# Kernel optimization log

Hardware: AMD Instinct MI355X
Metric: run time of the kernel (lower is better)

Reference implementation:

```python
import jax, jax.numpy as jnp
import numpy as np

LOG2 = float(np.log(2.0))

def ssp(v):
    # ShiftedSoftplus: softplus(x) - log(2)
    return jax.nn.softplus(v) - jnp.asarray(LOG2, v.dtype)

def setup_inputs() -> dict:
    key = jax.random.key(0)
    ks = jax.random.split(key, 16)
    N, B, F, R, P = 100000, 128, 64, 32, 1600000
    inp = {
        "x": jax.random.normal(ks[0], (N, B), jnp.float32),
        "f_ij": jax.random.uniform(ks[1], (P, R), jnp.float32),
        "rcut_ij": jax.random.uniform(ks[2], (P,), jnp.float32),
        "pairlist": jax.random.randint(ks[3], (2, P), 0, N, jnp.int64),
        # input_to_feature: Linear(B, F)
        "w_in": jax.random.normal(ks[4], (B, F), jnp.float32) * (1.0 / np.sqrt(B)),
        "b_in": jnp.zeros((F,), jnp.float32),
        # filter_network: Linear(R, F) + SSP, Linear(F, F)
        "w_f1": jax.random.normal(ks[5], (R, F), jnp.float32) * (1.0 / np.sqrt(R)),
        "b_f1": jnp.zeros((F,), jnp.float32),
        "w_f2": jax.random.normal(ks[6], (F, F), jnp.float32) * (1.0 / np.sqrt(F)),
        "b_f2": jnp.zeros((F,), jnp.float32),
        # feature_to_output: Linear(F, B) + SSP, Linear(B, B)
        "w_o1": jax.random.normal(ks[7], (F, B), jnp.float32) * (1.0 / np.sqrt(F)),
        "b_o1": jnp.zeros((B,), jnp.float32),
        "w_o2": jax.random.normal(ks[8], (B, B), jnp.float32) * (1.0 / np.sqrt(B)),
        "b_o2": jnp.zeros((B,), jnp.float32),
    }
    return inp

def reference(x, f_ij, rcut_ij, pairlist, w_in, b_in, w_f1, b_f1, w_f2, b_f2, w_o1, b_o1, w_o2, b_o2):
    n_atoms = x.shape[0]
    # input_to_feature
    h = x @ w_in + b_in                                    # [N, F]
    # filter_network on rbf features, weighted by cutoff
    Wij = ssp(f_ij @ w_f1 + b_f1) @ w_f2 + b_f2            # [P, F]
    Wij = Wij * rcut_ij[:, None]
    idx_i, idx_j = pairlist[0], pairlist[1]
    # gather neighbor features, modulate, scatter-add to center atoms
    x_ij = h[idx_j] * Wij                                  # [P, F]
    agg = jax.ops.segment_sum(x_ij, idx_i, num_segments=n_atoms)  # [N, F]
    # feature_to_output
    out = ssp(agg @ w_o1 + b_o1) @ w_o2 + b_o2             # [N, B]
    return out
```

## Files before the change

kernel.cpp:

```cpp
#include <hip/hip_runtime.h>
#include <hip/hip_bf16.h>
#include <hip/hip_fp16.h>

#define B_ 128
#define F_ 64
#define R_ 32

typedef __attribute__((ext_vector_type(8))) __bf16 bf16x8;
typedef __attribute__((ext_vector_type(4))) float f32x4;

#define LN2F 0.6931471805599453f
#define L2EF 1.4426950408889634f

__device__ __forceinline__ float sspf(float x) {
    float t = fabsf(x) * (-L2EF);
    float e; asm("v_exp_f32 %0, %1" : "=v"(e) : "v"(t));
    float l; asm("v_log_f32 %0, %1" : "=v"(l) : "v"(1.0f + e));
    return fmaxf(x, 0.0f) + fmaf(LN2F, l, -LN2F);
}
__device__ __forceinline__ float bfbits2f(unsigned int us) { return __uint_as_float(us << 16); }
__device__ __forceinline__ unsigned int f2bf(float f) {
    unsigned int u = __float_as_uint(f);
    return (u + 0x7fffu + ((u >> 16) & 1u)) >> 16;
}
__device__ __forceinline__ float h16f(unsigned short s) { return __half2float(__ushort_as_half(s)); }
__device__ __forceinline__ unsigned int pkbf(float a, float b) {
    __hip_bfloat162 h = __float22bfloat162_rn(make_float2(a, b));
    unsigned int r; __builtin_memcpy(&r, &h, 4); return r;
}
__device__ __forceinline__ unsigned int pkh(float a, float b) {
    __half2 h = __float22half2_rn(make_float2(a, b));
    unsigned int r; __builtin_memcpy(&r, &h, 4); return r;
}

__global__ __launch_bounds__(256) void front_kernel(
    const float* __restrict__ w1, const float* __restrict__ w2,
    const float* __restrict__ wo1, const float* __restrict__ wo2,
    unsigned short* __restrict__ w1p, unsigned short* __restrict__ w2p,
    unsigned short* __restrict__ wo1p, unsigned short* __restrict__ wo2p,
    const void* __restrict__ pl, int* __restrict__ flag, int P,
    const float* __restrict__ x, const float* __restrict__ w_in,
    const float* __restrict__ b_in, unsigned short* __restrict__ h, int NA,
    int* __restrict__ hist, int hgrid)
{
    int b = blockIdx.x;
    if (b < 15) {
        int t = b * 256 + threadIdx.x;
        if (t < 256) {
            int ct = t >> 6, l = t & 63, g = l >> 4, m = l & 15;
            #pragma unroll
            for (int i = 0; i < 8; ++i)
                w1p[t * 8 + i] = (unsigned short)f2bf(w1[(g * 8 + i) * F_ + ct * 16 + m]);
        } else if (t < 768) {
            int q = t - 256;
            int kh = q >> 8, ct = (q >> 6) & 3, l = q & 63, g = l >> 4, m = l & 15;
            #pragma unroll
            for (int i = 0; i < 8; ++i)
                w2p[q * 8 + i] = (unsigned short)f2bf(w2[(kh * 32 + g * 8 + i) * F_ + ct * 16 + m]);
        } else if (t < 2816) {
            int q = t - 768;
            int l = q & 63, ct = (q >> 6) & 3, kh = (q >> 8) & 3, ch = q >> 10;
            int g = l >> 4, m = l & 15;
            #pragma unroll
            for (int i = 0; i < 8; ++i)
                wo2p[q * 8 + i] = (unsigned short)f2bf(wo2[(kh * 32 + g * 8 + i) * B_ + ch * 64 + ct * 16 + m]);
        } else if (t < 3840) {
            int q = t - 2816;
            int l = q & 63, ct = (q >> 6) & 3, kh = (q >> 8) & 1, ch = q >> 9;
            int g = l >> 4, m = l & 15;
            #pragma unroll
            for (int i = 0; i < 8; ++i)
                wo1p[q * 8 + i] = (unsigned short)f2bf(wo1[(kh * 32 + g * 8 + i) * B_ + ch * 64 + ct * 16 + m]);
        }
        return;
    }
    if (b == 15) {
        if (threadIdx.x < 64) {
            int n = (P < 64) ? P : 64;
            const long long* p64 = (const long long*)pl;
            bool bad = false;
            if ((int)threadIdx.x < n) {
                long long v = p64[threadIdx.x];
                bad = (v < 0) || (v >= 100000000LL);
            }
            unsigned long long bl = __ballot(bad);
            if (threadIdx.x == 0) *flag = (bl == 0ULL) ? 1 : 0;
        }
        return;
    }
    if (b < 16 + hgrid) {
        int n = (b - 16) * 256 + threadIdx.x;
        if (n >= NA) return;
        float acc[F_];
        #pragma unroll
        for (int f = 0; f < F_; ++f) acc[f] = b_in[f];
        const float4* xrow = (const float4*)(x + (size_t)n * B_);
        #pragma unroll 2
        for (int rb = 0; rb < B_ / 4; ++rb) {
            float4 xv = xrow[rb];
            const float* w0 = w_in + (size_t)(4 * rb) * F_;
            #pragma unroll
            for (int f = 0; f < F_; ++f) acc[f] = fmaf(xv.x, w0[f], acc[f]);
            #pragma unroll
            for (int f = 0; f < F_; ++f) acc[f] = fmaf(xv.y, w0[F_ + f], acc[f]);
            #pragma unroll
            for (int f = 0; f < F_; ++f) acc[f] = fmaf(xv.z, w0[2 * F_ + f], acc[f]);
            #pragma unroll
            for (int f = 0; f < F_; ++f) acc[f] = fmaf(xv.w, w0[3 * F_ + f], acc[f]);
        }
        uint4* hrow = (uint4*)(h + (size_t)n * F_);
        #pragma unroll
        for (int q = 0; q < F_ / 8; ++q) {
            uint4 ob;
            ob.x = pkbf(acc[8 * q + 0], acc[8 * q + 1]);
            ob.y = pkbf(acc[8 * q + 2], acc[8 * q + 3]);
            ob.z = pkbf(acc[8 * q + 4], acc[8 * q + 5]);
            ob.w = pkbf(acc[8 * q + 6], acc[8 * q + 7]);
            hrow[q] = ob;
        }
        return;
    }
    __shared__ int sflag;
    if (threadIdx.x < 64) {
        int n = (P < 64) ? P : 64;
        const long long* p64 = (const long long*)pl;
        bool bad = false;
        if ((int)threadIdx.x < n) {
            long long v = p64[threadIdx.x];
            bad = (v < 0) || (v >= 100000000LL);
        }
        unsigned long long bl = __ballot(bad);
        if (threadIdx.x == 0) sflag = (bl == 0ULL) ? 1 : 0;
    }
    __syncthreads();
    int p = (b - 16 - hgrid) * 256 + threadIdx.x;
    if (p >= P) return;
    int i = sflag ? (int)((const long long*)pl)[p] : ((const int*)pl)[p];
    atomicAdd(&hist[i], 1);
}

__global__ __launch_bounds__(256) void scan1_kernel(
    const int* __restrict__ hist, int* __restrict__ off,
    int* __restrict__ bsum, int NA)
{
    __shared__ int s[256];
    int t = threadIdx.x;
    int idx = blockIdx.x * 2048 + t * 8;
    int v[8];
    int run = 0;
    #pragma unroll
    for (int k = 0; k < 8; ++k) {
        int i = idx + k;
        int c = (i < NA) ? hist[i] : 0;
        v[k] = run; run += c;
    }
    s[t] = run;
    __syncthreads();
    for (int o = 1; o < 256; o <<= 1) {
        int x = (t >= o) ? s[t - o] : 0;
        __syncthreads();
        s[t] += x;
        __syncthreads();
    }
    int base = (t == 0) ? 0 : s[t - 1];
    #pragma unroll
    for (int k = 0; k < 8; ++k) {
        int i = idx + k;
        if (i < NA) off[i] = v[k] + base;
    }
    if (t == 255) bsum[blockIdx.x] = s[255];
}

__global__ __launch_bounds__(256) void scan2_kernel(int* __restrict__ bsum, int nb) {
    __shared__ int s[256];
    int t = threadIdx.x;
    int v = (t < nb) ? bsum[t] : 0;
    s[t] = v;
    __syncthreads();
    for (int o = 1; o < 256; o <<= 1) {
        int x = (t >= o) ? s[t - o] : 0;
        __syncthreads();
        s[t] += x;
        __syncthreads();
    }
    if (t < nb) bsum[t] = s[t] - v;
}

__global__ __launch_bounds__(256) void scan3_kernel(
    int* __restrict__ off, int* __restrict__ cursor,
    const int* __restrict__ bsum, int NA, int P)
{
    int i = blockIdx.x * 256 + threadIdx.x;
    if (i > NA) return;
    if (i == NA) { off[NA] = P; return; }
    int v = off[i] + bsum[i >> 11];
    off[i] = v;
    cursor[i] = v;
}

template <bool ATOMIC>
__global__ __launch_bounds__(256, 4) void pair_kernel(
    const float* __restrict__ f_ij, const float* __restrict__ rcut,
    const void* __restrict__ pl, const int* __restrict__ flag,
    const unsigned short* __restrict__ w1p, const float* __restrict__ b1,
    const unsigned short* __restrict__ w2p, const float* __restrict__ b2,
    const unsigned short* __restrict__ h, unsigned short* __restrict__ xs,
    int* __restrict__ cursor, int* __restrict__ jslot,
    float* __restrict__ agg_f32, int P)
{
    __shared__ __align__(16) unsigned short T[256 * 64];
    __shared__ __align__(16) int   ii[256];
    __shared__ __align__(16) int   jj[256];
    __shared__ __align__(16) float rr[256];

    const int tid   = threadIdx.x;
    const int lane  = tid & 63;
    const int wv    = tid >> 6;
    const int g     = lane >> 4;
    const int m     = lane & 15;
    const int pbase = blockIdx.x * 256;
    const int wbase = wv * 64;

    {
        int p = pbase + tid;
        bool valid = (p < P);
        int pc = valid ? p : (P > 0 ? P - 1 : 0);
        long long i_, j_;
        if (*flag) {
            const long long* p64 = (const long long*)pl;
            i_ = p64[pc]; j_ = p64[(size_t)P + pc];
        } else {
            const int* p32 = (const int*)pl;
            i_ = p32[pc]; j_ = p32[(size_t)P + pc];
        }
        jj[tid] = valid ? (int)j_ : 0;
        rr[tid] = valid ? rcut[pc] : 0.0f;
        if (ATOMIC) {
            ii[tid] = valid ? (int)i_ : 0;
        } else {
            int pos = valid ? atomicAdd(&cursor[(int)i_], 1) : (P + tid);
            ii[tid] = pos;
            if (valid) jslot[pos] = (int)j_;
        }
    }

    bf16x8 w1f[4], w2f[2][4];
    #pragma unroll
    for (int ct = 0; ct < 4; ++ct)
        w1f[ct] = *(const bf16x8*)&w1p[(ct * 64 + lane) * 8];
    #pragma unroll
    for (int kh = 0; kh < 2; ++kh)
        #pragma unroll
        for (int ct = 0; ct < 4; ++ct)
            w2f[kh][ct] = *(const bf16x8*)&w2p[((kh * 4 + ct) * 64 + lane) * 8];

    float4 b1v[4], b2v[4];
    #pragma unroll
    for (int ft = 0; ft < 4; ++ft) {
        b1v[ft] = *(const float4*)&b1[ft * 16 + g * 4];
        b2v[ft] = *(const float4*)&b2[ft * 16 + g * 4];
    }

    bf16x8 fijf[4];
    #pragma unroll
    for (int pt = 0; pt < 4; ++pt) {
        int row = pbase + wbase + pt * 16 + m;
        if (row >= P) row = (P > 0 ? P - 1 : 0);
        const float* srcp = f_ij + (size_t)row * R_ + g * 8;
        float4 f0 = *(const float4*)srcp;
        float4 f1 = *(const float4*)(srcp + 4);
        uint4 pk;
        pk.x = pkbf(f0.x, f0.y);
        pk.y = pkbf(f0.z, f0.w);
        pk.z = pkbf(f1.x, f1.y);
        pk.w = pkbf(f1.z, f1.w);
        bf16x8 av; __builtin_memcpy(&av, &pk, 16);
        fijf[pt] = av;
    }
    f32x4 C1[4][4];
    #pragma unroll
    for (int ft = 0; ft < 4; ++ft)
        #pragma unroll
        for (int pt = 0; pt < 4; ++pt) {
            f32x4 z = {0.f, 0.f, 0.f, 0.f};
            C1[ft][pt] = __builtin_amdgcn_mfma_f32_16x16x32_bf16(w1f[ft], fijf[pt], z, 0, 0, 0);
        }

    #pragma unroll
    for (int ft = 0; ft < 4; ++ft)
        #pragma unroll
        for (int pt = 0; pt < 4; ++pt) {
            int wp = pt * 16 + m;
            float v0 = sspf(C1[ft][pt][0] + b1v[ft].x);
            float v1 = sspf(C1[ft][pt][1] + b1v[ft].y);
            float v2 = sspf(C1[ft][pt][2] + b1v[ft].z);
            float v3 = sspf(C1[ft][pt][3] + b1v[ft].w);
            uint2 tw;
            tw.x = pkbf(v0, v1);
            tw.y = pkbf(v2, v3);
            int c = (ft * 4 + g) ^ ((wp & 7) << 1);
            *(uint2*)&T[(wbase + wp) * 64 + c * 4] = tw;
        }

    #pragma unroll
    for (int pt = 0; pt < 4; ++pt) {
        int wpr = pt * 16 + m;
        int s = wpr & 7;
        const unsigned short* Trow = &T[(wbase + wpr) * 64];
        bf16x8 t0 = *(const bf16x8*)&Trow[((0 + g) ^ s) * 8];
        bf16x8 t1 = *(const bf16x8*)&Trow[((4 + g) ^ s) * 8];
        f32x4 C2f[4];
        #pragma unroll
        for (int ft = 0; ft < 4; ++ft) {
            f32x4 c = {0.f, 0.f, 0.f, 0.f};
            c = __builtin_amdgcn_mfma_f32_16x16x32_bf16(w2f[0][ft], t0, c, 0, 0, 0);
            c = __builtin_amdgcn_mfma_f32_16x16x32_bf16(w2f[1][ft], t1, c, 0, 0, 0);
            C2f[ft] = c;
        }

        int pp = wbase + pt * 16 + m;
        float rc = rr[pp];
        if (!ATOMIC) {
            unsigned short* xrow = xs + (size_t)ii[pp] * F_;
            #pragma unroll
            for (int ft = 0; ft < 4; ++ft) {
                int f0 = ft * 16 + g * 4;
                float x0 = (C2f[ft][0] + b2v[ft].x) * rc;
                float x1 = (C2f[ft][1] + b2v[ft].y) * rc;
                float x2 = (C2f[ft][2] + b2v[ft].z) * rc;
                float x3 = (C2f[ft][3] + b2v[ft].w) * rc;
                uint2 w;
                w.x = pkh(x0, x1);
                w.y = pkh(x2, x3);
                *(uint2*)&xrow[f0] = w;
            }
        } else {
            int j_ = jj[pp];
            const unsigned short* hrow = h + (size_t)j_ * F_;
            float* aggrow = agg_f32 + (size_t)ii[pp] * F_;
            #pragma unroll
            for (int ft = 0; ft < 4; ++ft) {
                int f0 = ft * 16 + g * 4;
                ushort4 hv = *(const ushort4*)&hrow[f0];
                atomicAdd(aggrow + f0 + 0, (C2f[ft][0] + b2v[ft].x) * rc * bfbits2f(hv.x));
                atomicAdd(aggrow + f0 + 1, (C2f[ft][1] + b2v[ft].y) * rc * bfbits2f(hv.y));
                atomicAdd(aggrow + f0 + 2, (C2f[ft][2] + b2v[ft].z) * rc * bfbits2f(hv.z));
                atomicAdd(aggrow + f0 + 3, (C2f[ft][3] + b2v[ft].w) * rc * bfbits2f(hv.w));
            }
        }
    }
}

__global__ __launch_bounds__(256) void reduce_kernel(
    const unsigned short* __restrict__ xs, const int* __restrict__ jslot,
    const int* __restrict__ off, const unsigned short* __restrict__ h,
    unsigned short* __restrict__ aggb, int NA)
{
    int a = blockIdx.x * 4 + (threadIdx.x >> 6);
    int lane = threadIdx.x & 63;
    if (a >= NA) return;
    int s = off[a], e = off[a + 1];
    float a0 = 0.f, a1 = 0.f, a2 = 0.f, a3 = 0.f;
    int k = s;
    for (; k + 4 <= e; k += 4) {
        int j0 = jslot[k + 0], j1 = jslot[k + 1];
        int j2 = jslot[k + 2], j3 = jslot[k + 3];
        float w0 = h16f(xs[(size_t)(k + 0) * F_ + lane]);
        float w1 = h16f(xs[(size_t)(k + 1) * F_ + lane]);
        float w2 = h16f(xs[(size_t)(k + 2) * F_ + lane]);
        float w3 = h16f(xs[(size_t)(k + 3) * F_ + lane]);
        float h0 = bfbits2f(h[(size_t)j0 * F_ + lane]);
        float h1 = bfbits2f(h[(size_t)j1 * F_ + lane]);
        float h2 = bfbits2f(h[(size_t)j2 * F_ + lane]);
        float h3 = bfbits2f(h[(size_t)j3 * F_ + lane]);
        a0 = fmaf(w0, h0, a0);
        a1 = fmaf(w1, h1, a1);
        a2 = fmaf(w2, h2, a2);
        a3 = fmaf(w3, h3, a3);
    }
    for (; k < e; ++k) {
        int j0 = jslot[k];
        a0 = fmaf(h16f(xs[(size_t)k * F_ + lane]),
                  bfbits2f(h[(size_t)j0 * F_ + lane]), a0);
    }
    aggb[(size_t)a * F_ + lane] = (unsigned short)f2bf((a0 + a1) + (a2 + a3));
}

template <bool AGGB>
__global__ __launch_bounds__(256) void out12_kernel(
    const void* __restrict__ agg_p,
    const unsigned short* __restrict__ wo1p, const float* __restrict__ b_o1,
    const unsigned short* __restrict__ wo2p, const float* __restrict__ b_o2,
    float* __restrict__ out, int NA)
{
    __shared__ __align__(16) unsigned short U[4][64][136];

    const int tid  = threadIdx.x;
    const int lane = tid & 63;
    const int wv   = tid >> 6;
    const int g    = lane >> 4;
    const int m    = lane & 15;
    const int rbase = blockIdx.x * 256 + wv * 64;

    {
        bf16x8 wf[2][2][4];
        #pragma unroll
        for (int ch = 0; ch < 2; ++ch)
            #pragma unroll
            for (int kh = 0; kh < 2; ++kh)
                #pragma unroll
                for (int ct = 0; ct < 4; ++ct)
                    wf[ch][kh][ct] = *(const bf16x8*)&wo1p[(((ch * 2 + kh) * 4 + ct) * 64 + lane) * 8];
        float4 bo1[2][4];
        #pragma unroll
        for (int ch = 0; ch < 2; ++ch)
            #pragma unroll
            for (int ct = 0; ct < 4; ++ct)
                bo1[ch][ct] = *(const float4*)&b_o1[ch * 64 + ct * 16 + g * 4];

        #pragma unroll
        for (int rt = 0; rt < 4; ++rt) {
            int row = rbase + rt * 16 + m;
            if (row >= NA) row = NA - 1;
            bf16x8 af[2];
            #pragma unroll
            for (int kh = 0; kh < 2; ++kh) {
                if (AGGB) {
                    af[kh] = *(const bf16x8*)((const unsigned short*)agg_p + (size_t)row * F_ + kh * 32 + g * 8);
                } else {
                    const float* ar = (const float*)agg_p + (size_t)row * F_ + kh * 32 + g * 8;
                    float4 v0 = *(const float4*)ar;
                    float4 v1 = *(const float4*)(ar + 4);
                    uint4 pk;
                    pk.x = pkbf(v0.x, v0.y); pk.y = pkbf(v0.z, v0.w);
                    pk.z = pkbf(v1.x, v1.y); pk.w = pkbf(v1.z, v1.w);
                    bf16x8 av; __builtin_memcpy(&av, &pk, 16);
                    af[kh] = av;
                }
            }
            #pragma unroll
            for (int ch = 0; ch < 2; ++ch)
                #pragma unroll
                for (int ct = 0; ct < 4; ++ct) {
                    f32x4 c = {0.f, 0.f, 0.f, 0.f};
                    c = __builtin_amdgcn_mfma_f32_16x16x32_bf16(wf[ch][0][ct], af[0], c, 0, 0, 0);
                    c = __builtin_amdgcn_mfma_f32_16x16x32_bf16(wf[ch][1][ct], af[1], c, 0, 0, 0);
                    float u0 = sspf(c[0] + bo1[ch][ct].x);
                    float u1 = sspf(c[1] + bo1[ch][ct].y);
                    float u2 = sspf(c[2] + bo1[ch][ct].z);
                    float u3 = sspf(c[3] + bo1[ch][ct].w);
                    uint2 uw;
                    uw.x = pkbf(u0, u1);
                    uw.y = pkbf(u2, u3);
                    *(uint2*)&U[wv][rt * 16 + m][ch * 64 + ct * 16 + g * 4] = uw;
                }
        }
    }

    #pragma unroll
    for (int ch = 0; ch < 2; ++ch) {
        bf16x8 wf2[4][4];
        #pragma unroll
        for (int kh = 0; kh < 4; ++kh)
            #pragma unroll
            for (int ct = 0; ct < 4; ++ct)
                wf2[kh][ct] = *(const bf16x8*)&wo2p[(((ch * 4 + kh) * 4 + ct) * 64 + lane) * 8];
        float bo2[4];
        #pragma unroll
        for (int ct = 0; ct < 4; ++ct) bo2[ct] = b_o2[ch * 64 + ct * 16 + m];

        #pragma unroll
        for (int rt = 0; rt < 4; ++rt) {
            bf16x8 af[4];
            #pragma unroll
            for (int kh = 0; kh < 4; ++kh)
                af[kh] = *(const bf16x8*)&U[wv][rt * 16 + m][kh * 32 + g * 8];
            #pragma unroll
            for (int ct = 0; ct < 4; ++ct) {
                f32x4 c = {0.f, 0.f, 0.f, 0.f};
                #pragma unroll
                for (int kh = 0; kh < 4; ++kh)
                    c = __builtin_amdgcn_mfma_f32_16x16x32_bf16(af[kh], wf2[kh][ct], c, 0, 0, 0);
                #pragma unroll
                for (int r = 0; r < 4; ++r) {
                    int ro = rbase + rt * 16 + g * 4 + r;
                    if (ro < NA)
                        out[(size_t)ro * B_ + ch * 64 + ct * 16 + m] = c[r] + bo2[ct];
                }
            }
        }
    }
}

extern "C" void kernel_launch(void* const* d_in, const int* in_sizes, int n_in,
                              void* d_out, int out_size, void* d_ws, size_t ws_size,
                              hipStream_t stream) {
    const float* x    = (const float*)d_in[0];
    const float* f_ij = (const float*)d_in[1];
    const float* rcut = (const float*)d_in[2];
    const void*  pl   = d_in[3];
    const float* w_in = (const float*)d_in[4];
    const float* b_in = (const float*)d_in[5];
    const float* w_f1 = (const float*)d_in[6];
    const float* b_f1 = (const float*)d_in[7];
    const float* w_f2 = (const float*)d_in[8];
    const float* b_f2 = (const float*)d_in[9];
    const float* w_o1 = (const float*)d_in[10];
    const float* b_o1 = (const float*)d_in[11];
    const float* w_o2 = (const float*)d_in[12];
    const float* b_o2 = (const float*)d_in[13];
    float* out = (float*)d_out;

    int NA = in_sizes[0] / B_;
    int P  = in_sizes[2];
    int nb = (NA + 2047) / 2048;
    int hgrid = (NA + 255) / 256;
    int pgrid = (P + 255) / 256;

    size_t hB    = (size_t)NA * F_ * 2;
    size_t xsB   = (size_t)(P + 256) * F_ * 2;
    size_t agB   = (size_t)NA * F_ * 2;
    size_t histB = (size_t)NA * 4;
    size_t offB  = (size_t)(NA + 1) * 4;
    size_t curB  = (size_t)NA * 4;
    size_t jsB   = (size_t)(P + 256) * 4;
    size_t wAll  = (2048 + 4096 + 8192 + 16384) * 2;
    size_t mainNeed = hB + xsB + agB + histB + offB + curB + jsB + 1024 + wAll + 8192;

    bool CSR = (ws_size >= mainNeed) && (nb <= 256);

    char* ws = (char*)d_ws;
    size_t off_ = 0;
    auto alloc = [&](size_t bytes) { size_t o = off_; off_ = (off_ + bytes + 255) & ~(size_t)255; return o; };

    unsigned short* h_buf = (unsigned short*)(ws + alloc(hB));
    unsigned short* w1p   = (unsigned short*)(ws + alloc(2048 * 2));
    unsigned short* w2p   = (unsigned short*)(ws + alloc(4096 * 2));
    unsigned short* wo1p  = (unsigned short*)(ws + alloc(8192 * 2));
    unsigned short* wo2p  = (unsigned short*)(ws + alloc(16384 * 2));
    int* flag             = (int*)(ws + alloc(256));

    if (CSR) {
        unsigned short* xs   = (unsigned short*)(ws + alloc(xsB));
        unsigned short* aggb = (unsigned short*)(ws + alloc(agB));
        int* hist            = (int*)(ws + alloc(histB));
        int* off             = (int*)(ws + alloc(offB));
        int* cursor          = (int*)(ws + alloc(curB));
        int* jslot           = (int*)(ws + alloc(jsB));
        int* bsum            = (int*)(ws + alloc(1024));

        (void)hipMemsetAsync(hist, 0, histB, stream);
        front_kernel<<<16 + hgrid + pgrid, 256, 0, stream>>>(
            w_f1, w_f2, w_o1, w_o2, w1p, w2p, wo1p, wo2p,
            pl, flag, P, x, w_in, b_in, h_buf, NA, hist, hgrid);
        scan1_kernel<<<nb, 256, 0, stream>>>(hist, off, bsum, NA);
        scan2_kernel<<<1, 256, 0, stream>>>(bsum, nb);
        scan3_kernel<<<(NA + 1 + 255) / 256, 256, 0, stream>>>(off, cursor, bsum, NA, P);
        pair_kernel<false><<<pgrid, 256, 0, stream>>>(
            f_ij, rcut, pl, flag, w1p, b_f1, w2p, b_f2, h_buf, xs, cursor, jslot, nullptr, P);
        reduce_kernel<<<(NA + 3) / 4, 256, 0, stream>>>(xs, jslot, off, h_buf, aggb, NA);
        out12_kernel<true><<<hgrid, 256, 0, stream>>>(aggb, wo1p, b_o1, wo2p, b_o2, out, NA);
    } else {
        float* agg = (float*)(ws + alloc((size_t)NA * F_ * 4));
        (void)hipMemsetAsync(agg, 0, (size_t)NA * F_ * 4, stream);
        front_kernel<<<16 + hgrid, 256, 0, stream>>>(
            w_f1, w_f2, w_o1, w_o2, w1p, w2p, wo1p, wo2p,
            pl, flag, P, x, w_in, b_in, h_buf, NA, nullptr, hgrid);
        pair_kernel<true><<<pgrid, 256, 0, stream>>>(
            f_ij, rcut, pl, flag, w1p, b_f1, w2p, b_f2, h_buf, nullptr, nullptr, nullptr, agg, P);
        out12_kernel<false><<<hgrid, 256, 0, stream>>>(agg, wo1p, b_o1, wo2p, b_o2, out, NA);
    }
}
```

Baseline: 409.9 us.

## Split CSR scatter into separate kernel and write pair outputs in original order

A new scatter kernel performs the atomic cursor increments and writes (pair index, neighbor index) metadata into CSR order. The pair kernel then writes its filter outputs coalesced at the original pair index instead of scattering rows to CSR slots. The reduce kernel reads xs indirectly through the metadata, which makes its xs reads random gathers. The goal is to turn scattered 128-byte row writes into coalesced writes, at the cost of an extra kernel launch, an extra pass over the pairlist and gathered reads in the reduce step.

```diff
diff --git a/kernel.cpp b/kernel.cpp
--- a/kernel.cpp
+++ b/kernel.cpp
@@ -198,6 +198,24 @@
     cursor[i] = v;
 }
 
+__global__ __launch_bounds__(256) void scatter_kernel(
+    const void* __restrict__ pl, const int* __restrict__ flag,
+    int* __restrict__ cursor, int2* __restrict__ meta, int P)
+{
+    int p = blockIdx.x * 256 + threadIdx.x;
+    if (p >= P) return;
+    int i, j;
+    if (*flag) {
+        const long long* q = (const long long*)pl;
+        i = (int)q[p]; j = (int)q[(size_t)P + p];
+    } else {
+        const int* q = (const int*)pl;
+        i = q[p]; j = q[(size_t)P + p];
+    }
+    int pos = atomicAdd(&cursor[i], 1);
+    meta[pos] = make_int2(p, j);
+}
+
 template <bool ATOMIC>
 __global__ __launch_bounds__(256, 4) void pair_kernel(
     const float* __restrict__ f_ij, const float* __restrict__ rcut,
@@ -205,7 +223,6 @@
     const unsigned short* __restrict__ w1p, const float* __restrict__ b1,
     const unsigned short* __restrict__ w2p, const float* __restrict__ b2,
     const unsigned short* __restrict__ h, unsigned short* __restrict__ xs,
-    int* __restrict__ cursor, int* __restrict__ jslot,
     float* __restrict__ agg_f32, int P)
 {
     __shared__ __align__(16) unsigned short T[256 * 64];
@@ -225,22 +242,18 @@
         int p = pbase + tid;
         bool valid = (p < P);
         int pc = valid ? p : (P > 0 ? P - 1 : 0);
-        long long i_, j_;
-        if (*flag) {
-            const long long* p64 = (const long long*)pl;
-            i_ = p64[pc]; j_ = p64[(size_t)P + pc];
-        } else {
-            const int* p32 = (const int*)pl;
-            i_ = p32[pc]; j_ = p32[(size_t)P + pc];
-        }
-        jj[tid] = valid ? (int)j_ : 0;
         rr[tid] = valid ? rcut[pc] : 0.0f;
         if (ATOMIC) {
+            long long i_, j_;
+            if (*flag) {
+                const long long* p64 = (const long long*)pl;
+                i_ = p64[pc]; j_ = p64[(size_t)P + pc];
+            } else {
+                const int* p32 = (const int*)pl;
+                i_ = p32[pc]; j_ = p32[(size_t)P + pc];
+            }
             ii[tid] = valid ? (int)i_ : 0;
-        } else {
-            int pos = valid ? atomicAdd(&cursor[(int)i_], 1) : (P + tid);
-            ii[tid] = pos;
-            if (valid) jslot[pos] = (int)j_;
+            jj[tid] = valid ? (int)j_ : 0;
         }
     }
 
@@ -319,20 +332,23 @@
         }
 
         int pp = wbase + pt * 16 + m;
+        int p  = pbase + pp;
         float rc = rr[pp];
         if (!ATOMIC) {
-            unsigned short* xrow = xs + (size_t)ii[pp] * F_;
-            #pragma unroll
-            for (int ft = 0; ft < 4; ++ft) {
-                int f0 = ft * 16 + g * 4;
-                float x0 = (C2f[ft][0] + b2v[ft].x) * rc;
-                float x1 = (C2f[ft][1] + b2v[ft].y) * rc;
-                float x2 = (C2f[ft][2] + b2v[ft].z) * rc;
-                float x3 = (C2f[ft][3] + b2v[ft].w) * rc;
-                uint2 w;
-                w.x = pkh(x0, x1);
-                w.y = pkh(x2, x3);
-                *(uint2*)&xrow[f0] = w;
+            if (p < P) {
+                unsigned short* xrow = xs + (size_t)p * F_;
+                #pragma unroll
+                for (int ft = 0; ft < 4; ++ft) {
+                    int f0 = ft * 16 + g * 4;
+                    float x0 = (C2f[ft][0] + b2v[ft].x) * rc;
+                    float x1 = (C2f[ft][1] + b2v[ft].y) * rc;
+                    float x2 = (C2f[ft][2] + b2v[ft].z) * rc;
+                    float x3 = (C2f[ft][3] + b2v[ft].w) * rc;
+                    uint2 w;
+                    w.x = pkh(x0, x1);
+                    w.y = pkh(x2, x3);
+                    *(uint2*)&xrow[f0] = w;
+                }
             }
         } else {
             int j_ = jj[pp];
@@ -352,7 +368,7 @@
 }
 
 __global__ __launch_bounds__(256) void reduce_kernel(
-    const unsigned short* __restrict__ xs, const int* __restrict__ jslot,
+    const unsigned short* __restrict__ xs, const int2* __restrict__ meta,
     const int* __restrict__ off, const unsigned short* __restrict__ h,
     unsigned short* __restrict__ aggb, int NA)
 {
@@ -363,25 +379,25 @@
     float a0 = 0.f, a1 = 0.f, a2 = 0.f, a3 = 0.f;
     int k = s;
     for (; k + 4 <= e; k += 4) {
-        int j0 = jslot[k + 0], j1 = jslot[k + 1];
-        int j2 = jslot[k + 2], j3 = jslot[k + 3];
-        float w0 = h16f(xs[(size_t)(k + 0) * F_ + lane]);
-        float w1 = h16f(xs[(size_t)(k + 1) * F_ + lane]);
-        float w2 = h16f(xs[(size_t)(k + 2) * F_ + lane]);
-        float w3 = h16f(xs[(size_t)(k + 3) * F_ + lane]);
-        float h0 = bfbits2f(h[(size_t)j0 * F_ + lane]);
-        float h1 = bfbits2f(h[(size_t)j1 * F_ + lane]);
-        float h2 = bfbits2f(h[(size_t)j2 * F_ + lane]);
-        float h3 = bfbits2f(h[(size_t)j3 * F_ + lane]);
+        int2 m0 = meta[k + 0], m1 = meta[k + 1];
+        int2 m2 = meta[k + 2], m3 = meta[k + 3];
+        float w0 = h16f(xs[(size_t)m0.x * F_ + lane]);
+        float w1 = h16f(xs[(size_t)m1.x * F_ + lane]);
+        float w2 = h16f(xs[(size_t)m2.x * F_ + lane]);
+        float w3 = h16f(xs[(size_t)m3.x * F_ + lane]);
+        float h0 = bfbits2f(h[(size_t)m0.y * F_ + lane]);
+        float h1 = bfbits2f(h[(size_t)m1.y * F_ + lane]);
+        float h2 = bfbits2f(h[(size_t)m2.y * F_ + lane]);
+        float h3 = bfbits2f(h[(size_t)m3.y * F_ + lane]);
         a0 = fmaf(w0, h0, a0);
         a1 = fmaf(w1, h1, a1);
         a2 = fmaf(w2, h2, a2);
         a3 = fmaf(w3, h3, a3);
     }
     for (; k < e; ++k) {
-        int j0 = jslot[k];
-        a0 = fmaf(h16f(xs[(size_t)k * F_ + lane]),
-                  bfbits2f(h[(size_t)j0 * F_ + lane]), a0);
+        int2 mk = meta[k];
+        a0 = fmaf(h16f(xs[(size_t)mk.x * F_ + lane]),
+                  bfbits2f(h[(size_t)mk.y * F_ + lane]), a0);
     }
     aggb[(size_t)a * F_ + lane] = (unsigned short)f2bf((a0 + a1) + (a2 + a3));
 }
@@ -523,9 +539,9 @@
     size_t histB = (size_t)NA * 4;
     size_t offB  = (size_t)(NA + 1) * 4;
     size_t curB  = (size_t)NA * 4;
-    size_t jsB   = (size_t)(P + 256) * 4;
+    size_t mtB   = (size_t)(P + 256) * 8;
     size_t wAll  = (2048 + 4096 + 8192 + 16384) * 2;
-    size_t mainNeed = hB + xsB + agB + histB + offB + curB + jsB + 1024 + wAll + 8192;
+    size_t mainNeed = hB + xsB + agB + histB + offB + curB + mtB + 1024 + wAll + 8192;
 
     bool CSR = (ws_size >= mainNeed) && (nb <= 256);
 
@@ -546,7 +562,7 @@
         int* hist            = (int*)(ws + alloc(histB));
         int* off             = (int*)(ws + alloc(offB));
         int* cursor          = (int*)(ws + alloc(curB));
-        int* jslot           = (int*)(ws + alloc(jsB));
+        int2* meta           = (int2*)(ws + alloc(mtB));
         int* bsum            = (int*)(ws + alloc(1024));
 
         (void)hipMemsetAsync(hist, 0, histB, stream);
@@ -556,9 +572,10 @@
         scan1_kernel<<<nb, 256, 0, stream>>>(hist, off, bsum, NA);
         scan2_kernel<<<1, 256, 0, stream>>>(bsum, nb);
         scan3_kernel<<<(NA + 1 + 255) / 256, 256, 0, stream>>>(off, cursor, bsum, NA, P);
+        scatter_kernel<<<pgrid, 256, 0, stream>>>(pl, flag, cursor, meta, P);
         pair_kernel<false><<<pgrid, 256, 0, stream>>>(
-            f_ij, rcut, pl, flag, w1p, b_f1, w2p, b_f2, h_buf, xs, cursor, jslot, nullptr, P);
-        reduce_kernel<<<(NA + 3) / 4, 256, 0, stream>>>(xs, jslot, off, h_buf, aggb, NA);
+            f_ij, rcut, pl, flag, w1p, b_f1, w2p, b_f2, h_buf, xs, nullptr, P);
+        reduce_kernel<<<(NA + 3) / 4, 256, 0, stream>>>(xs, meta, off, h_buf, aggb, NA);
         out12_kernel<true><<<hgrid, 256, 0, stream>>>(aggb, wo1p, b_o1, wo2p, b_o2, out, NA);
     } else {
         float* agg = (float*)(ws + alloc((size_t)NA * F_ * 4));
@@ -567,7 +584,7 @@
             w_f1, w_f2, w_o1, w_o2, w1p, w2p, wo1p, wo2p,
             pl, flag, P, x, w_in, b_in, h_buf, NA, nullptr, hgrid);
         pair_kernel<true><<<pgrid, 256, 0, stream>>>(
-            f_ij, rcut, pl, flag, w1p, b_f1, w2p, b_f2, h_buf, nullptr, nullptr, nullptr, agg, P);
+            f_ij, rcut, pl, flag, w1p, b_f1, w2p, b_f2, h_buf, nullptr, agg, P);
         out12_kernel<false><<<hgrid, 256, 0, stream>>>(agg, wo1p, b_o1, wo2p, b_o2, out, NA);
     }
 }
```

Measured after the change: 483.0 us. +17.8%, slower.
